# Kernel tuning notes

Measured on AMD Instinct MI355X. Metric: run time of the kernel, lower is better.

The kernel has to match this reference:

```python
import jax, jax.numpy as jnp
import numpy as np

D_MODEL = 768
D_FF = 2048
N_EXP = 8
TOP_K = 2


def setup_inputs() -> dict:
    key = jax.random.key(0)
    ks = jax.random.split(key, 8)
    s = 0.02
    inputs = jax.random.normal(ks[0], (4, 2048, D_MODEL), dtype=jnp.float32)
    gate_w = jax.random.normal(ks[1], (D_MODEL, N_EXP), dtype=jnp.float32) * s
    w1 = jax.random.normal(ks[2], (N_EXP, D_MODEL, D_FF), dtype=jnp.float32) * s
    w3 = jax.random.normal(ks[3], (N_EXP, D_MODEL, D_FF), dtype=jnp.float32) * s
    w2 = jax.random.normal(ks[4], (N_EXP, D_FF, D_MODEL), dtype=jnp.float32) * s
    sw1 = jax.random.normal(ks[5], (D_MODEL, D_FF), dtype=jnp.float32) * s
    sw3 = jax.random.normal(ks[6], (D_MODEL, D_FF), dtype=jnp.float32) * s
    sw2 = jax.random.normal(ks[7], (D_FF, D_MODEL), dtype=jnp.float32) * s
    return {"inputs": inputs, "gate_w": gate_w, "w1": w1, "w3": w3, "w2": w2,
            "sw1": sw1, "sw3": sw3, "sw2": sw2}


def _swiglu(x, wa, wb, wc):
    # silu(x @ wa) * (x @ wb) @ wc
    return (jax.nn.silu(x @ wa) * (x @ wb)) @ wc


def reference(inputs, gate_w, w1, w3, w2, sw1, sw3, sw2):
    B, T, D = inputs.shape
    x = inputs.reshape(-1, D)                      # [N, D], N = B*T
    logits = x @ gate_w                            # [N, E]
    topk_scores, topk_idx = jax.lax.top_k(logits, TOP_K)  # [N, K]
    probs = jax.nn.softmax(topk_scores.astype(jnp.float32), axis=-1).astype(inputs.dtype)
    # per-token per-expert combine weight: [N, E]
    one_hot = jax.nn.one_hot(topk_idx, N_EXP, dtype=probs.dtype)  # [N, K, E]
    comb = jnp.einsum('nk,nke->ne', probs, one_hot)               # [N, E]
    out = jnp.zeros_like(x)
    for e in range(N_EXP):  # fixed small expert loop
        out = out + comb[:, e:e + 1] * _swiglu(x, w1[e], w3[e], w2[e])
    out = out + _swiglu(x, sw1, sw3, sw2)
    return out.reshape(B, T, D)
```

## Files before the change

kernel.cpp:

```cpp
#include <hip/hip_runtime.h>
#include <hip/hip_bf16.h>

#define N_TOK 8192
#define DM 768
#define DFF 2048
#define NE 8
#define SHARED_BASE 17408
#define TOTAL_ROWS 25600

typedef __attribute__((ext_vector_type(8))) __bf16 bf16x8;
typedef __attribute__((ext_vector_type(4))) float f32x4;

__device__ __forceinline__ unsigned short f2bf(float f) {
  union { float f; unsigned u; } a; a.f = f;
  unsigned r = a.u + 0x7FFFu + ((a.u >> 16) & 1u);
  return (unsigned short)(r >> 16);
}

__device__ __forceinline__ void gload16(const void* g, void* l) {
  __builtin_amdgcn_global_load_lds((const __attribute__((address_space(1))) void*)g,
                                   (__attribute__((address_space(3))) void*)l, 16, 0, 0);
}


__global__ void cvt_x_kernel(const float4* __restrict__ src, ushort4* __restrict__ dst, int n4) {
  int stride = gridDim.x * blockDim.x;
  for (int i = blockIdx.x * blockDim.x + threadIdx.x; i < n4; i += stride) {
    float4 v = src[i];
    ushort4 o;
    o.x = f2bf(v.x); o.y = f2bf(v.y); o.z = f2bf(v.z); o.w = f2bf(v.w);
    dst[i] = o;
  }
}

__global__ void transpose_cvt_kernel(const float* __restrict__ src, unsigned short* __restrict__ dst,
                                     int R, int C) {
  __shared__ float tile[64][65];
  const float* s = src + (size_t)blockIdx.z * R * C;
  unsigned short* d = dst + (size_t)blockIdx.z * R * C;
  int c0 = blockIdx.x * 64, r0 = blockIdx.y * 64;
  int tx = threadIdx.x & 63, ty = threadIdx.x >> 6;
#pragma unroll
  for (int i = 0; i < 16; i++) {
    int row = i * 4 + ty;
    tile[row][tx] = s[(size_t)(r0 + row) * C + c0 + tx];
  }
  __syncthreads();
#pragma unroll
  for (int i = 0; i < 16; i++) {
    int row = i * 4 + ty;
    d[(size_t)(c0 + row) * R + r0 + tx] = f2bf(tile[tx][row]);
  }
}

__global__ __launch_bounds__(256) void gate_kernel(
    const float* __restrict__ x, const float* __restrict__ gw,
    float* __restrict__ probs, int* __restrict__ idxo) {
  __shared__ float gws[8][768];
  const int tid = threadIdx.x;
  for (int i = tid; i < DM * 2; i += 256) {
    float4 v = ((const float4*)gw)[i];
    int dd = i >> 1;
    int e0 = (i & 1) * 4;
    gws[e0 + 0][dd] = v.x; gws[e0 + 1][dd] = v.y;
    gws[e0 + 2][dd] = v.z; gws[e0 + 3][dd] = v.w;
  }
  __syncthreads();
  const int lane = tid & 63, wv = tid >> 6;
  const int tok0 = blockIdx.x * 16 + wv * 4;
  for (int i = 0; i < 4; i++) {
    const int n = tok0 + i;
    const float* xr = x + (size_t)n * DM;
    float xv[12];
#pragma unroll
    for (int it = 0; it < 12; it++) xv[it] = xr[it * 64 + lane];
    double acc[8];
#pragma unroll
    for (int e = 0; e < 8; e++) {
      double a = 0.0;
#pragma unroll
      for (int it = 0; it < 12; it++) a += (double)xv[it] * (double)gws[e][it * 64 + lane];
      acc[e] = a;
    }
#pragma unroll
    for (int off = 32; off > 0; off >>= 1)
#pragma unroll
      for (int e = 0; e < 8; e++) acc[e] += __shfl_xor(acc[e], off);
    if (lane == 0) {
      int e0 = 0; double v0 = acc[0];
#pragma unroll
      for (int e = 1; e < 8; e++) if (acc[e] > v0) { v0 = acc[e]; e0 = e; }
      int e1 = -1; double v1 = -1e300;
#pragma unroll
      for (int e = 0; e < 8; e++) if (e != e0 && acc[e] > v1) { v1 = acc[e]; e1 = e; }
      double p0 = 1.0 / (1.0 + exp(v1 - v0));
      probs[n * 2 + 0] = (float)p0;
      probs[n * 2 + 1] = (float)(1.0 - p0);
      idxo[n * 2 + 0] = e0;
      idxo[n * 2 + 1] = e1;
    }
  }
}

__global__ __launch_bounds__(256) void route_kernel(
    const int* __restrict__ idxo, const float* __restrict__ probs,
    int* __restrict__ cnt, int* __restrict__ offs,
    int* __restrict__ list, float* __restrict__ pslot) {
  __shared__ int lcnt[256][8];
  __shared__ int lstart[256][8];
  __shared__ int base[8];
  const int t = threadIdx.x;
#pragma unroll
  for (int e = 0; e < 8; e++) lcnt[t][e] = 0;
  __syncthreads();
  const int i0 = t * 64;
  for (int j = 0; j < 64; j++) {
    int e = idxo[i0 + j];
    lcnt[t][e]++;
  }
  __syncthreads();
  if (t < 8) {
    int run = 0;
    for (int tt = 0; tt < 256; tt++) { lstart[tt][t] = run; run += lcnt[tt][t]; }
    base[t] = run;
  }
  __syncthreads();
  if (t == 0) {
    int cum = 0;
    for (int e = 0; e < 8; e++) {
      int tot = base[e];
      cnt[e] = tot; offs[e] = cum;
      base[e] = cum;
      cum += (tot + 127) & ~127;
    }
    offs[8] = cum;
  }
  __syncthreads();
#pragma unroll
  for (int e = 0; e < 8; e++) lcnt[t][e] = base[e] + lstart[t][e];
  for (int j = 0; j < 64; j++) {
    int i = i0 + j;
    int e = idxo[i];
    int pos = lcnt[t][e]++;
    list[pos] = i >> 1;
    pslot[pos] = probs[i];
  }
}

__global__ __launch_bounds__(256, 2) void gemm1_kernel(
    const char* __restrict__ xb,
    const char* __restrict__ w1T,
    const char* __restrict__ w3T,
    const char* __restrict__ sw1T,
    const char* __restrict__ sw3T,
    const int* __restrict__ list, const int* __restrict__ cnt, const int* __restrict__ offs,
    unsigned short* __restrict__ Hb)
{
  __shared__ unsigned short Al[128 * 64];
  __shared__ unsigned short B1l[64 * 64];
  __shared__ unsigned short B3l[64 * 64];

  const int by = blockIdx.y;
  const int f0 = blockIdx.x * 64;
  const int tid = threadIdx.x;
  const int lane = tid & 63;
  const int wv = tid >> 6;
  const int wm = wv >> 1, wn = wv & 1;
  const int wflat = tid & ~63;

  const char *w1p, *w3p;
  int base_slot, tbase, cnt_e, offs_e = 0;
  const bool is_shared = (by >= 512);
  if (!is_shared) {
    int e = by >> 6, t = by & 63;
    cnt_e = cnt[e];
    if (t * 128 >= cnt_e) return;
    offs_e = offs[e];
    base_slot = offs_e + t * 128;
    tbase = t * 128;
    w1p = w1T + (size_t)e * DFF * DM * 2;
    w3p = w3T + (size_t)e * DFF * DM * 2;
  } else {
    int t = by - 512;
    base_slot = SHARED_BASE + t * 128;
    tbase = t * 128;
    cnt_e = 1 << 30;
    w1p = sw1T; w3p = sw3T;
  }

  const int brow = tid >> 3;
  const int bcol = tid & 7;

  size_t abase[4];
#pragma unroll
  for (int it = 0; it < 4; it++) {
    int row = it * 32 + brow;
    int tok;
    if (is_shared) tok = tbase + row;
    else {
      int ie = tbase + row;
      if (ie >= cnt_e) ie = cnt_e - 1;
      tok = list[offs_e + ie];
    }
    abase[it] = (size_t)tok * (DM * 2) + (size_t)((bcol ^ (row & 7)) << 4);
  }
  size_t bbase[2];
#pragma unroll
  for (int it = 0; it < 2; it++) {
    int row = it * 32 + brow;
    bbase[it] = (size_t)(f0 + row) * (DM * 2) + (size_t)((bcol ^ (row & 7)) << 4);
  }

  f32x4 acc1[4][2], acc3[4][2];
  const f32x4 z4 = {0.f, 0.f, 0.f, 0.f};
#pragma unroll
  for (int mi = 0; mi < 4; mi++)
#pragma unroll
    for (int ni = 0; ni < 2; ni++) { acc1[mi][ni] = z4; acc3[mi][ni] = z4; }

  const int ml = lane & 15, kg = lane >> 4;

  for (int ks = 0; ks < 12; ks++) {
#pragma unroll
    for (int it = 0; it < 4; it++)
      gload16(xb + abase[it] + ks * 128, (char*)Al + (size_t)((it * 256 + wflat) * 16));
#pragma unroll
    for (int it = 0; it < 2; it++) {
      gload16(w1p + bbase[it] + ks * 128, (char*)B1l + (size_t)((it * 256 + wflat) * 16));
      gload16(w3p + bbase[it] + ks * 128, (char*)B3l + (size_t)((it * 256 + wflat) * 16));
    }
    __syncthreads();
#pragma unroll
    for (int kk = 0; kk < 2; kk++) {
      const int kblk = kk * 4 + kg;
      bf16x8 af[4], b1f[2], b3f[2];
#pragma unroll
      for (int mi = 0; mi < 4; mi++) {
        int m = wm * 64 + mi * 16 + ml;
        af[mi] = *(const bf16x8*)((const char*)Al + m * 128 + ((kblk ^ (ml & 7)) << 4));
      }
#pragma unroll
      for (int ni = 0; ni < 2; ni++) {
        int nn = wn * 32 + ni * 16 + ml;
        int boff = nn * 128 + ((kblk ^ (ml & 7)) << 4);
        b1f[ni] = *(const bf16x8*)((const char*)B1l + boff);
        b3f[ni] = *(const bf16x8*)((const char*)B3l + boff);
      }
#pragma unroll
      for (int mi = 0; mi < 4; mi++)
#pragma unroll
        for (int ni = 0; ni < 2; ni++) {
          acc1[mi][ni] = __builtin_amdgcn_mfma_f32_16x16x32_bf16(af[mi], b1f[ni], acc1[mi][ni], 0, 0, 0);
          acc3[mi][ni] = __builtin_amdgcn_mfma_f32_16x16x32_bf16(af[mi], b3f[ni], acc3[mi][ni], 0, 0, 0);
        }
    }
    __syncthreads();
  }

#pragma unroll
  for (int mi = 0; mi < 4; mi++) {
#pragma unroll
    for (int ni = 0; ni < 2; ni++) {
#pragma unroll
      for (int r = 0; r < 4; r++) {
        int row = wm * 64 + mi * 16 + (lane >> 4) * 4 + r;
        int col = f0 + wn * 32 + ni * 16 + ml;
        float h1 = acc1[mi][ni][r], h3 = acc3[mi][ni][r];
        float s = h1 / (1.0f + expf(-h1));
        Hb[(size_t)(base_slot + row) * DFF + col] = f2bf(s * h3);
      }
    }
  }
}

__global__ __launch_bounds__(256, 2) void gemm2_kernel(
    const char* __restrict__ Hb,
    const char* __restrict__ w2T,
    const char* __restrict__ sw2T,
    const int* __restrict__ list, const int* __restrict__ cnt, const int* __restrict__ offs,
    const float* __restrict__ pslot,
    float* __restrict__ out, int shared_pass)
{
  __shared__ unsigned short Al[128 * 64];
  __shared__ unsigned short Bl[128 * 64];

  const int by = blockIdx.y;
  const int d0 = blockIdx.x * 128;
  const int tid = threadIdx.x;
  const int lane = tid & 63;
  const int wv = tid >> 6;
  const int wm = wv >> 1, wn = wv & 1;
  const int wflat = tid & ~63;

  const char* w2p;
  int base_slot, offs_e = 0, tbase, cnt_e;
  if (!shared_pass) {
    int e = by >> 6, t = by & 63;
    cnt_e = cnt[e];
    if (t * 128 >= cnt_e) return;
    offs_e = offs[e];
    base_slot = offs_e + t * 128;
    tbase = t * 128;
    w2p = w2T + (size_t)e * DM * DFF * 2;
  } else {
    int t = by;
    base_slot = SHARED_BASE + t * 128;
    tbase = t * 128;
    cnt_e = 1 << 30;
    w2p = sw2T;
  }

  const int brow = tid >> 3, bcol = tid & 7;
  size_t abase[4], bbase[4];
#pragma unroll
  for (int it = 0; it < 4; it++) {
    int row = it * 32 + brow;
    abase[it] = (size_t)(base_slot + row) * (DFF * 2) + (size_t)((bcol ^ (row & 7)) << 4);
    bbase[it] = (size_t)(d0 + row) * (DFF * 2) + (size_t)((bcol ^ (row & 7)) << 4);
  }

  f32x4 acc[4][4];
  const f32x4 z4 = {0.f, 0.f, 0.f, 0.f};
#pragma unroll
  for (int mi = 0; mi < 4; mi++)
#pragma unroll
    for (int ni = 0; ni < 4; ni++) acc[mi][ni] = z4;

  const int ml = lane & 15, kg = lane >> 4;

  for (int ks = 0; ks < 32; ks++) {
#pragma unroll
    for (int it = 0; it < 4; it++) {
      gload16(Hb + abase[it] + ks * 128, (char*)Al + (size_t)((it * 256 + wflat) * 16));
      gload16(w2p + bbase[it] + ks * 128, (char*)Bl + (size_t)((it * 256 + wflat) * 16));
    }
    __syncthreads();
#pragma unroll
    for (int kk = 0; kk < 2; kk++) {
      const int kblk = kk * 4 + kg;
      bf16x8 af[4], bf[4];
#pragma unroll
      for (int mi = 0; mi < 4; mi++) {
        int m = wm * 64 + mi * 16 + ml;
        af[mi] = *(const bf16x8*)((const char*)Al + m * 128 + ((kblk ^ (ml & 7)) << 4));
      }
#pragma unroll
      for (int ni = 0; ni < 4; ni++) {
        int nn = wn * 64 + ni * 16 + ml;
        bf[ni] = *(const bf16x8*)((const char*)Bl + nn * 128 + ((kblk ^ (ml & 7)) << 4));
      }
#pragma unroll
      for (int mi = 0; mi < 4; mi++)
#pragma unroll
        for (int ni = 0; ni < 4; ni++)
          acc[mi][ni] = __builtin_amdgcn_mfma_f32_16x16x32_bf16(af[mi], bf[ni], acc[mi][ni], 0, 0, 0);
    }
    __syncthreads();
  }

#pragma unroll
  for (int mi = 0; mi < 4; mi++) {
#pragma unroll
    for (int r = 0; r < 4; r++) {
      int row = wm * 64 + mi * 16 + (lane >> 4) * 4 + r;
      int ie = tbase + row;
      if (!shared_pass && ie >= cnt_e) continue;
      int tok; float p;
      if (shared_pass) { tok = tbase + row; p = 1.0f; }
      else { int slot = offs_e + ie; tok = list[slot]; p = pslot[slot]; }
      float* orow = out + (size_t)tok * DM + d0;
#pragma unroll
      for (int ni = 0; ni < 4; ni++) {
        int col = wn * 64 + ni * 16 + ml;
        float v = p * acc[mi][ni][r];
        if (shared_pass) orow[col] = v;
        else atomicAdd(&orow[col], v);
      }
    }
  }
}


extern "C" void kernel_launch(void* const* d_in, const int* in_sizes, int n_in,
                              void* d_out, int out_size, void* d_ws, size_t ws_size,
                              hipStream_t stream) {
  const float* x   = (const float*)d_in[0];
  const float* gw  = (const float*)d_in[1];
  const float* w1  = (const float*)d_in[2];
  const float* w3  = (const float*)d_in[3];
  const float* w2  = (const float*)d_in[4];
  const float* sw1 = (const float*)d_in[5];
  const float* sw3 = (const float*)d_in[6];
  const float* sw2 = (const float*)d_in[7];
  float* out = (float*)d_out;
  char* ws = (char*)d_ws;

  char* xb    = ws;
  char* w1T   = xb    + 12582912;
  char* w3T   = w1T   + 25165824;
  char* w2T   = w3T   + 25165824;
  char* sw1T  = w2T   + 25165824;
  char* sw3T  = sw1T  + 3145728;
  char* sw2T  = sw3T  + 3145728;
  char* Hb    = sw2T  + 3145728;
  char* probs = Hb    + 104857600;
  char* idxo  = probs + 65536;
  char* lst   = idxo  + 65536;
  char* psl   = lst   + 69632;
  char* cntb  = psl   + 69632;
  char* curb  = cntb  + 64;
  char* offb  = curb  + 64;

  cvt_x_kernel<<<2048, 256, 0, stream>>>((const float4*)x, (ushort4*)xb, N_TOK * DM / 4);
  transpose_cvt_kernel<<<dim3(32, 12, 8), 256, 0, stream>>>(w1, (unsigned short*)w1T, DM, DFF);
  transpose_cvt_kernel<<<dim3(32, 12, 8), 256, 0, stream>>>(w3, (unsigned short*)w3T, DM, DFF);
  transpose_cvt_kernel<<<dim3(12, 32, 8), 256, 0, stream>>>(w2, (unsigned short*)w2T, DFF, DM);
  transpose_cvt_kernel<<<dim3(32, 12, 1), 256, 0, stream>>>(sw1, (unsigned short*)sw1T, DM, DFF);
  transpose_cvt_kernel<<<dim3(32, 12, 1), 256, 0, stream>>>(sw3, (unsigned short*)sw3T, DM, DFF);
  transpose_cvt_kernel<<<dim3(12, 32, 1), 256, 0, stream>>>(sw2, (unsigned short*)sw2T, DFF, DM);

  gate_kernel<<<512, 256, 0, stream>>>(x, gw, (float*)probs, (int*)idxo);
  route_kernel<<<1, 256, 0, stream>>>((const int*)idxo, (const float*)probs,
                                      (int*)cntb, (int*)offb, (int*)lst, (float*)psl);

  gemm1_kernel<<<dim3(32, 576), 256, 0, stream>>>(xb, w1T, w3T, sw1T, sw3T,
      (const int*)lst, (const int*)cntb, (const int*)offb, (unsigned short*)Hb);

  gemm2_kernel<<<dim3(6, 64), 256, 0, stream>>>(Hb, w2T, sw2T, (const int*)lst, (const int*)cntb,
      (const int*)offb, (const float*)psl, out, 1);
  gemm2_kernel<<<dim3(6, 512), 256, 0, stream>>>(Hb, w2T, sw2T, (const int*)lst, (const int*)cntb,
      (const int*)offb, (const float*)psl, out, 0);
}
```

Measured before the change: 440.7 us.

## Enlarge GEMM tiles to 512 threads, double-buffer LDS, merge shared-expert pass

```diff
diff --git a/kernel.cpp b/kernel.cpp
--- a/kernel.cpp
+++ b/kernel.cpp
@@ -147,7 +147,7 @@
   }
 }
 
-__global__ __launch_bounds__(256, 2) void gemm1_kernel(
+__global__ __launch_bounds__(512, 2) void gemm1_kernel(
     const char* __restrict__ xb,
     const char* __restrict__ w1T,
     const char* __restrict__ w3T,
@@ -156,45 +156,44 @@
     const int* __restrict__ list, const int* __restrict__ cnt, const int* __restrict__ offs,
     unsigned short* __restrict__ Hb)
 {
-  __shared__ unsigned short Al[128 * 64];
-  __shared__ unsigned short B1l[64 * 64];
-  __shared__ unsigned short B3l[64 * 64];
+  __shared__ __attribute__((aligned(128))) unsigned char lds[131072];
 
   const int by = blockIdx.y;
-  const int f0 = blockIdx.x * 64;
+  const int f0 = blockIdx.x * 128;
   const int tid = threadIdx.x;
   const int lane = tid & 63;
   const int wv = tid >> 6;
-  const int wm = wv >> 1, wn = wv & 1;
-  const int wflat = tid & ~63;
+  const int wm = wv >> 1;
+  const int wn = wv & 1;
+  const int ml = lane & 15, kg = lane >> 4;
 
   const char *w1p, *w3p;
-  int base_slot, tbase, cnt_e, offs_e = 0;
-  const bool is_shared = (by >= 512);
+  int base_slot, tbase, cnt_e, cnt_pad = 1 << 30, offs_e = 0;
+  const bool is_shared = (by >= 256);
   if (!is_shared) {
-    int e = by >> 6, t = by & 63;
+    int e = by >> 5, t = by & 31;
     cnt_e = cnt[e];
-    if (t * 128 >= cnt_e) return;
+    if (t * 256 >= cnt_e) return;
+    cnt_pad = (cnt_e + 127) & ~127;
     offs_e = offs[e];
-    base_slot = offs_e + t * 128;
-    tbase = t * 128;
+    base_slot = offs_e + t * 256;
+    tbase = t * 256;
     w1p = w1T + (size_t)e * DFF * DM * 2;
     w3p = w3T + (size_t)e * DFF * DM * 2;
   } else {
-    int t = by - 512;
-    base_slot = SHARED_BASE + t * 128;
-    tbase = t * 128;
+    int t = by - 256;
+    base_slot = SHARED_BASE + t * 256;
+    tbase = t * 256;
     cnt_e = 1 << 30;
     w1p = sw1T; w3p = sw3T;
   }
 
-  const int brow = tid >> 3;
-  const int bcol = tid & 7;
-
+  const int srow = tid >> 3;
+  const int schk = tid & 7;
   size_t abase[4];
 #pragma unroll
   for (int it = 0; it < 4; it++) {
-    int row = it * 32 + brow;
+    int row = it * 64 + srow;
     int tok;
     if (is_shared) tok = tbase + row;
     else {
@@ -202,121 +201,130 @@
       if (ie >= cnt_e) ie = cnt_e - 1;
       tok = list[offs_e + ie];
     }
-    abase[it] = (size_t)tok * (DM * 2) + (size_t)((bcol ^ (row & 7)) << 4);
-  }
-  size_t bbase[2];
-#pragma unroll
-  for (int it = 0; it < 2; it++) {
-    int row = it * 32 + brow;
-    bbase[it] = (size_t)(f0 + row) * (DM * 2) + (size_t)((bcol ^ (row & 7)) << 4);
-  }
-
-  f32x4 acc1[4][2], acc3[4][2];
+    abase[it] = (size_t)tok * (DM * 2) + (size_t)((schk ^ (row & 7)) << 4);
+  }
+  const char* bptr[4];
+#pragma unroll
+  for (int it = 0; it < 4; it++) {
+    const char* wp = (it & 1) ? w3p : w1p;
+    int frow = f0 + ((it >> 1) << 6) + srow;
+    bptr[it] = wp + (size_t)frow * (DM * 2) + (size_t)((schk ^ (srow & 7)) << 4);
+  }
+
+  f32x4 acc[4][8];
   const f32x4 z4 = {0.f, 0.f, 0.f, 0.f};
 #pragma unroll
   for (int mi = 0; mi < 4; mi++)
 #pragma unroll
-    for (int ni = 0; ni < 2; ni++) { acc1[mi][ni] = z4; acc3[mi][ni] = z4; }
-
-  const int ml = lane & 15, kg = lane >> 4;
-
+    for (int nj = 0; nj < 8; nj++) acc[mi][nj] = z4;
+
+#define G1_STAGE(ks, b) {                                                        \
+    char* Ab_ = (char*)lds + (b) * 65536;                                        \
+    char* Bb_ = Ab_ + 32768;                                                     \
+    _Pragma("unroll")                                                            \
+    for (int it = 0; it < 4; it++)                                               \
+      gload16(xb + abase[it] + (ks) * 128, Ab_ + (it * 512 + tid) * 16);         \
+    _Pragma("unroll")                                                            \
+    for (int it = 0; it < 4; it++)                                               \
+      gload16(bptr[it] + (ks) * 128, Bb_ + (it * 512 + tid) * 16);               \
+  }
+
+  G1_STAGE(0, 0);
+  __syncthreads();
+  int cur = 0;
   for (int ks = 0; ks < 12; ks++) {
-#pragma unroll
-    for (int it = 0; it < 4; it++)
-      gload16(xb + abase[it] + ks * 128, (char*)Al + (size_t)((it * 256 + wflat) * 16));
-#pragma unroll
-    for (int it = 0; it < 2; it++) {
-      gload16(w1p + bbase[it] + ks * 128, (char*)B1l + (size_t)((it * 256 + wflat) * 16));
-      gload16(w3p + bbase[it] + ks * 128, (char*)B3l + (size_t)((it * 256 + wflat) * 16));
-    }
-    __syncthreads();
+    if (ks < 11) G1_STAGE(ks + 1, cur ^ 1);
+    const char* Ab = (const char*)lds + cur * 65536;
+    const char* Bb = Ab + 32768;
 #pragma unroll
     for (int kk = 0; kk < 2; kk++) {
       const int kblk = kk * 4 + kg;
-      bf16x8 af[4], b1f[2], b3f[2];
-#pragma unroll
-      for (int mi = 0; mi < 4; mi++) {
-        int m = wm * 64 + mi * 16 + ml;
-        af[mi] = *(const bf16x8*)((const char*)Al + m * 128 + ((kblk ^ (ml & 7)) << 4));
+      const int chk = (kblk ^ (ml & 7)) << 4;
+      bf16x8 af[4], bfr[8];
+#pragma unroll
+      for (int mi = 0; mi < 4; mi++)
+        af[mi] = *(const bf16x8*)(Ab + (wm * 64 + mi * 16 + ml) * 128 + chk);
+#pragma unroll
+      for (int nj = 0; nj < 8; nj++)
+        bfr[nj] = *(const bf16x8*)(Bb + (wn * 128 + nj * 16 + ml) * 128 + chk);
+#pragma unroll
+      for (int mi = 0; mi < 4; mi++)
+#pragma unroll
+        for (int nj = 0; nj < 8; nj++)
+          acc[mi][nj] = __builtin_amdgcn_mfma_f32_16x16x32_bf16(af[mi], bfr[nj], acc[mi][nj], 0, 0, 0);
+    }
+    __syncthreads();
+    cur ^= 1;
+  }
+
+#pragma unroll
+  for (int mi = 0; mi < 4; mi++) {
+#pragma unroll
+    for (int r = 0; r < 4; r++) {
+      int row = wm * 64 + mi * 16 + (lane >> 4) * 4 + r;
+      if (!is_shared && tbase + row >= cnt_pad) continue;
+      size_t hrow = (size_t)(base_slot + row) * DFF;
+#pragma unroll
+      for (int nj = 0; nj < 4; nj++) {
+        float h1 = acc[mi][nj][r], h3 = acc[mi][nj + 4][r];
+        float s = h1 / (1.0f + expf(-h1));
+        Hb[hrow + f0 + wn * 64 + nj * 16 + ml] = f2bf(s * h3);
       }
-#pragma unroll
-      for (int ni = 0; ni < 2; ni++) {
-        int nn = wn * 32 + ni * 16 + ml;
-        int boff = nn * 128 + ((kblk ^ (ml & 7)) << 4);
-        b1f[ni] = *(const bf16x8*)((const char*)B1l + boff);
-        b3f[ni] = *(const bf16x8*)((const char*)B3l + boff);
-      }
-#pragma unroll
-      for (int mi = 0; mi < 4; mi++)
-#pragma unroll
-        for (int ni = 0; ni < 2; ni++) {
-          acc1[mi][ni] = __builtin_amdgcn_mfma_f32_16x16x32_bf16(af[mi], b1f[ni], acc1[mi][ni], 0, 0, 0);
-          acc3[mi][ni] = __builtin_amdgcn_mfma_f32_16x16x32_bf16(af[mi], b3f[ni], acc3[mi][ni], 0, 0, 0);
-        }
-    }
-    __syncthreads();
-  }
-
-#pragma unroll
-  for (int mi = 0; mi < 4; mi++) {
-#pragma unroll
-    for (int ni = 0; ni < 2; ni++) {
-#pragma unroll
-      for (int r = 0; r < 4; r++) {
-        int row = wm * 64 + mi * 16 + (lane >> 4) * 4 + r;
-        int col = f0 + wn * 32 + ni * 16 + ml;
-        float h1 = acc1[mi][ni][r], h3 = acc3[mi][ni][r];
-        float s = h1 / (1.0f + expf(-h1));
-        Hb[(size_t)(base_slot + row) * DFF + col] = f2bf(s * h3);
-      }
-    }
-  }
-}
-
-__global__ __launch_bounds__(256, 2) void gemm2_kernel(
+    }
+  }
+#undef G1_STAGE
+}
+
+__global__ __launch_bounds__(512, 2) void gemm2_kernel(
     const char* __restrict__ Hb,
     const char* __restrict__ w2T,
     const char* __restrict__ sw2T,
     const int* __restrict__ list, const int* __restrict__ cnt, const int* __restrict__ offs,
     const float* __restrict__ pslot,
-    float* __restrict__ out, int shared_pass)
+    float* __restrict__ out)
 {
-  __shared__ unsigned short Al[128 * 64];
-  __shared__ unsigned short Bl[128 * 64];
+  __shared__ __attribute__((aligned(128))) unsigned char lds[98304];
 
   const int by = blockIdx.y;
   const int d0 = blockIdx.x * 128;
   const int tid = threadIdx.x;
   const int lane = tid & 63;
   const int wv = tid >> 6;
-  const int wm = wv >> 1, wn = wv & 1;
-  const int wflat = tid & ~63;
+  const int wm = wv >> 1;
+  const int wn = wv & 1;
+  const int ml = lane & 15, kg = lane >> 4;
 
   const char* w2p;
   int base_slot, offs_e = 0, tbase, cnt_e;
-  if (!shared_pass) {
-    int e = by >> 6, t = by & 63;
+  const bool is_shared = (by >= 256);
+  if (!is_shared) {
+    int e = by >> 5, t = by & 31;
     cnt_e = cnt[e];
-    if (t * 128 >= cnt_e) return;
+    if (t * 256 >= cnt_e) return;
     offs_e = offs[e];
-    base_slot = offs_e + t * 128;
-    tbase = t * 128;
+    base_slot = offs_e + t * 256;
+    tbase = t * 256;
     w2p = w2T + (size_t)e * DM * DFF * 2;
   } else {
-    int t = by;
-    base_slot = SHARED_BASE + t * 128;
-    tbase = t * 128;
+    int t = by - 256;
+    base_slot = SHARED_BASE + t * 256;
+    tbase = t * 256;
     cnt_e = 1 << 30;
     w2p = sw2T;
   }
 
-  const int brow = tid >> 3, bcol = tid & 7;
-  size_t abase[4], bbase[4];
+  const int srow = tid >> 3, schk = tid & 7;
+  size_t abase[4];
 #pragma unroll
   for (int it = 0; it < 4; it++) {
-    int row = it * 32 + brow;
-    abase[it] = (size_t)(base_slot + row) * (DFF * 2) + (size_t)((bcol ^ (row & 7)) << 4);
-    bbase[it] = (size_t)(d0 + row) * (DFF * 2) + (size_t)((bcol ^ (row & 7)) << 4);
+    int row = it * 64 + srow;
+    abase[it] = (size_t)(base_slot + row) * (DFF * 2) + (size_t)((schk ^ (row & 7)) << 4);
+  }
+  size_t bbase[2];
+#pragma unroll
+  for (int it = 0; it < 2; it++) {
+    int row = it * 64 + srow;
+    bbase[it] = (size_t)(d0 + row) * (DFF * 2) + (size_t)((schk ^ (row & 7)) << 4);
   }
 
   f32x4 acc[4][4];
@@ -324,38 +332,45 @@
 #pragma unroll
   for (int mi = 0; mi < 4; mi++)
 #pragma unroll
-    for (int ni = 0; ni < 4; ni++) acc[mi][ni] = z4;
-
-  const int ml = lane & 15, kg = lane >> 4;
-
+    for (int nj = 0; nj < 4; nj++) acc[mi][nj] = z4;
+
+#define G2_STAGE(ks, b) {                                                        \
+    char* Ab_ = (char*)lds + (b) * 49152;                                        \
+    char* Bb_ = Ab_ + 32768;                                                     \
+    _Pragma("unroll")                                                            \
+    for (int it = 0; it < 4; it++)                                               \
+      gload16(Hb + abase[it] + (ks) * 128, Ab_ + (it * 512 + tid) * 16);         \
+    _Pragma("unroll")                                                            \
+    for (int it = 0; it < 2; it++)                                               \
+      gload16(w2p + bbase[it] + (ks) * 128, Bb_ + (it * 512 + tid) * 16);        \
+  }
+
+  G2_STAGE(0, 0);
+  __syncthreads();
+  int cur = 0;
   for (int ks = 0; ks < 32; ks++) {
-#pragma unroll
-    for (int it = 0; it < 4; it++) {
-      gload16(Hb + abase[it] + ks * 128, (char*)Al + (size_t)((it * 256 + wflat) * 16));
-      gload16(w2p + bbase[it] + ks * 128, (char*)Bl + (size_t)((it * 256 + wflat) * 16));
-    }
-    __syncthreads();
+    if (ks < 31) G2_STAGE(ks + 1, cur ^ 1);
+    const char* Ab = (const char*)lds + cur * 49152;
+    const char* Bb = Ab + 32768;
 #pragma unroll
     for (int kk = 0; kk < 2; kk++) {
       const int kblk = kk * 4 + kg;
-      bf16x8 af[4], bf[4];
-#pragma unroll
-      for (int mi = 0; mi < 4; mi++) {
-        int m = wm * 64 + mi * 16 + ml;
-        af[mi] = *(const bf16x8*)((const char*)Al + m * 128 + ((kblk ^ (ml & 7)) << 4));
-      }
-#pragma unroll
-      for (int ni = 0; ni < 4; ni++) {
-        int nn = wn * 64 + ni * 16 + ml;
-        bf[ni] = *(const bf16x8*)((const char*)Bl + nn * 128 + ((kblk ^ (ml & 7)) << 4));
-      }
+      const int chk = (kblk ^ (ml & 7)) << 4;
+      bf16x8 af[4], bfr[4];
 #pragma unroll
       for (int mi = 0; mi < 4; mi++)
-#pragma unroll
-        for (int ni = 0; ni < 4; ni++)
-          acc[mi][ni] = __builtin_amdgcn_mfma_f32_16x16x32_bf16(af[mi], bf[ni], acc[mi][ni], 0, 0, 0);
+        af[mi] = *(const bf16x8*)(Ab + (wm * 64 + mi * 16 + ml) * 128 + chk);
+#pragma unroll
+      for (int nj = 0; nj < 4; nj++)
+        bfr[nj] = *(const bf16x8*)(Bb + (wn * 64 + nj * 16 + ml) * 128 + chk);
+#pragma unroll
+      for (int mi = 0; mi < 4; mi++)
+#pragma unroll
+        for (int nj = 0; nj < 4; nj++)
+          acc[mi][nj] = __builtin_amdgcn_mfma_f32_16x16x32_bf16(af[mi], bfr[nj], acc[mi][nj], 0, 0, 0);
     }
     __syncthreads();
+    cur ^= 1;
   }
 
 #pragma unroll
@@ -364,20 +379,17 @@
     for (int r = 0; r < 4; r++) {
       int row = wm * 64 + mi * 16 + (lane >> 4) * 4 + r;
       int ie = tbase + row;
-      if (!shared_pass && ie >= cnt_e) continue;
+      if (!is_shared && ie >= cnt_e) continue;
       int tok; float p;
-      if (shared_pass) { tok = tbase + row; p = 1.0f; }
+      if (is_shared) { tok = tbase + row; p = 1.0f; }
       else { int slot = offs_e + ie; tok = list[slot]; p = pslot[slot]; }
       float* orow = out + (size_t)tok * DM + d0;
 #pragma unroll
-      for (int ni = 0; ni < 4; ni++) {
-        int col = wn * 64 + ni * 16 + ml;
-        float v = p * acc[mi][ni][r];
-        if (shared_pass) orow[col] = v;
-        else atomicAdd(&orow[col], v);
-      }
-    }
-  }
+      for (int nj = 0; nj < 4; nj++)
+        atomicAdd(&orow[wn * 64 + nj * 16 + ml], p * acc[mi][nj][r]);
+    }
+  }
+#undef G2_STAGE
 }
 
 
@@ -408,8 +420,9 @@
   char* lst   = idxo  + 65536;
   char* psl   = lst   + 69632;
   char* cntb  = psl   + 69632;
-  char* curb  = cntb  + 64;
-  char* offb  = curb  + 64;
+  char* offb  = cntb  + 64;
+
+  (void)hipMemsetAsync(out, 0, (size_t)out_size * 4, stream);
 
   cvt_x_kernel<<<2048, 256, 0, stream>>>((const float4*)x, (ushort4*)xb, N_TOK * DM / 4);
   transpose_cvt_kernel<<<dim3(32, 12, 8), 256, 0, stream>>>(w1, (unsigned short*)w1T, DM, DFF);
@@ -423,11 +436,9 @@
   route_kernel<<<1, 256, 0, stream>>>((const int*)idxo, (const float*)probs,
                                       (int*)cntb, (int*)offb, (int*)lst, (float*)psl);
 
-  gemm1_kernel<<<dim3(32, 576), 256, 0, stream>>>(xb, w1T, w3T, sw1T, sw3T,
+  gemm1_kernel<<<dim3(16, 288), 512, 0, stream>>>(xb, w1T, w3T, sw1T, sw3T,
       (const int*)lst, (const int*)cntb, (const int*)offb, (unsigned short*)Hb);
 
-  gemm2_kernel<<<dim3(6, 64), 256, 0, stream>>>(Hb, w2T, sw2T, (const int*)lst, (const int*)cntb,
-      (const int*)offb, (const float*)psl, out, 1);
-  gemm2_kernel<<<dim3(6, 512), 256, 0, stream>>>(Hb, w2T, sw2T, (const int*)lst, (const int*)cntb,
-      (const int*)offb, (const float*)psl, out, 0);
-}
+  gemm2_kernel<<<dim3(6, 288), 512, 0, stream>>>(Hb, w2T, sw2T, (const int*)lst, (const int*)cntb,
+      (const int*)offb, (const float*)psl, out);
+}
```

Result: slower. 458.4 us (+4.0%).

## Replace atomic scatter in expert down-projection with slot buffer plus combine kernel

Applied to the files above, without the earlier changes.

```diff
diff --git a/kernel.cpp b/kernel.cpp
--- a/kernel.cpp
+++ b/kernel.cpp
@@ -103,9 +103,9 @@
 }
 
 __global__ __launch_bounds__(256) void route_kernel(
-    const int* __restrict__ idxo, const float* __restrict__ probs,
+    const int* __restrict__ idxo,
     int* __restrict__ cnt, int* __restrict__ offs,
-    int* __restrict__ list, float* __restrict__ pslot) {
+    int* __restrict__ list, int* __restrict__ slt) {
   __shared__ int lcnt[256][8];
   __shared__ int lstart[256][8];
   __shared__ int base[8];
@@ -143,7 +143,7 @@
     int e = idxo[i];
     int pos = lcnt[t][e]++;
     list[pos] = i >> 1;
-    pslot[pos] = probs[i];
+    slt[i] = pos;
   }
 }
 
@@ -277,9 +277,9 @@
     const char* __restrict__ Hb,
     const char* __restrict__ w2T,
     const char* __restrict__ sw2T,
-    const int* __restrict__ list, const int* __restrict__ cnt, const int* __restrict__ offs,
-    const float* __restrict__ pslot,
-    float* __restrict__ out, int shared_pass)
+    const int* __restrict__ cnt, const int* __restrict__ offs,
+    float* __restrict__ Ob,
+    float* __restrict__ out)
 {
   __shared__ unsigned short Al[128 * 64];
   __shared__ unsigned short Bl[128 * 64];
@@ -293,17 +293,17 @@
   const int wflat = tid & ~63;
 
   const char* w2p;
-  int base_slot, offs_e = 0, tbase, cnt_e;
-  if (!shared_pass) {
+  int base_slot, tbase, cnt_e;
+  const bool is_shared = (by >= 512);
+  if (!is_shared) {
     int e = by >> 6, t = by & 63;
     cnt_e = cnt[e];
     if (t * 128 >= cnt_e) return;
-    offs_e = offs[e];
-    base_slot = offs_e + t * 128;
+    base_slot = offs[e] + t * 128;
     tbase = t * 128;
     w2p = w2T + (size_t)e * DM * DFF * 2;
   } else {
-    int t = by;
+    int t = by - 512;
     base_slot = SHARED_BASE + t * 128;
     tbase = t * 128;
     cnt_e = 1 << 30;
@@ -338,7 +338,7 @@
 #pragma unroll
     for (int kk = 0; kk < 2; kk++) {
       const int kblk = kk * 4 + kg;
-      bf16x8 af[4], bf[4];
+      bf16x8 af[4], bfr[4];
 #pragma unroll
       for (int mi = 0; mi < 4; mi++) {
         int m = wm * 64 + mi * 16 + ml;
@@ -347,13 +347,13 @@
 #pragma unroll
       for (int ni = 0; ni < 4; ni++) {
         int nn = wn * 64 + ni * 16 + ml;
-        bf[ni] = *(const bf16x8*)((const char*)Bl + nn * 128 + ((kblk ^ (ml & 7)) << 4));
+        bfr[ni] = *(const bf16x8*)((const char*)Bl + nn * 128 + ((kblk ^ (ml & 7)) << 4));
       }
 #pragma unroll
       for (int mi = 0; mi < 4; mi++)
 #pragma unroll
         for (int ni = 0; ni < 4; ni++)
-          acc[mi][ni] = __builtin_amdgcn_mfma_f32_16x16x32_bf16(af[mi], bf[ni], acc[mi][ni], 0, 0, 0);
+          acc[mi][ni] = __builtin_amdgcn_mfma_f32_16x16x32_bf16(af[mi], bfr[ni], acc[mi][ni], 0, 0, 0);
     }
     __syncthreads();
   }
@@ -363,21 +363,30 @@
 #pragma unroll
     for (int r = 0; r < 4; r++) {
       int row = wm * 64 + mi * 16 + (lane >> 4) * 4 + r;
-      int ie = tbase + row;
-      if (!shared_pass && ie >= cnt_e) continue;
-      int tok; float p;
-      if (shared_pass) { tok = tbase + row; p = 1.0f; }
-      else { int slot = offs_e + ie; tok = list[slot]; p = pslot[slot]; }
-      float* orow = out + (size_t)tok * DM + d0;
-#pragma unroll
-      for (int ni = 0; ni < 4; ni++) {
-        int col = wn * 64 + ni * 16 + ml;
-        float v = p * acc[mi][ni][r];
-        if (shared_pass) orow[col] = v;
-        else atomicAdd(&orow[col], v);
-      }
-    }
-  }
+      float* orow = is_shared ? (out + (size_t)(tbase + row) * DM + d0)
+                              : (Ob + (size_t)(base_slot + row) * DM + d0);
+#pragma unroll
+      for (int ni = 0; ni < 4; ni++)
+        orow[wn * 64 + ni * 16 + ml] = acc[mi][ni][r];
+    }
+  }
+}
+
+__global__ __launch_bounds__(192) void combine_kernel(
+    const float4* __restrict__ Ob4, const int* __restrict__ slt,
+    const float* __restrict__ probs, float4* __restrict__ out4) {
+  const int n = blockIdx.x;
+  const int t = threadIdx.x;
+  const int s0 = slt[2 * n], s1 = slt[2 * n + 1];
+  const float p0 = probs[2 * n], p1 = probs[2 * n + 1];
+  float4 a = out4[(size_t)n * 192 + t];
+  float4 b = Ob4[(size_t)s0 * 192 + t];
+  float4 c = Ob4[(size_t)s1 * 192 + t];
+  a.x += p0 * b.x + p1 * c.x;
+  a.y += p0 * b.y + p1 * c.y;
+  a.z += p0 * b.z + p1 * c.z;
+  a.w += p0 * b.w + p1 * c.w;
+  out4[(size_t)n * 192 + t] = a;
 }
 
 
@@ -395,21 +404,22 @@
   float* out = (float*)d_out;
   char* ws = (char*)d_ws;
 
-  char* xb    = ws;
-  char* w1T   = xb    + 12582912;
-  char* w3T   = w1T   + 25165824;
-  char* w2T   = w3T   + 25165824;
-  char* sw1T  = w2T   + 25165824;
-  char* sw3T  = sw1T  + 3145728;
-  char* sw2T  = sw3T  + 3145728;
-  char* Hb    = sw2T  + 3145728;
-  char* probs = Hb    + 104857600;
-  char* idxo  = probs + 65536;
-  char* lst   = idxo  + 65536;
-  char* psl   = lst   + 69632;
-  char* cntb  = psl   + 69632;
-  char* curb  = cntb  + 64;
-  char* offb  = curb  + 64;
+  char* xb   = ws;
+  char* w2T  = xb + 12582912;
+  char* sw2T = w2T + 25165824;
+  char* U    = sw2T + 3145728;
+  char* w1T  = U;
+  char* w3T  = w1T + 25165824;
+  char* sw1T = w3T + 25165824;
+  char* sw3T = sw1T + 3145728;
+  char* Ob   = U;
+  char* Hb   = U + 56623104;
+  char* probs= Hb + 104857600;
+  char* idxo = probs + 65536;
+  char* lst  = idxo + 65536;
+  char* slt  = lst + 69632;
+  char* cntb = slt + 69632;
+  char* offb = cntb + 64;
 
   cvt_x_kernel<<<2048, 256, 0, stream>>>((const float4*)x, (ushort4*)xb, N_TOK * DM / 4);
   transpose_cvt_kernel<<<dim3(32, 12, 8), 256, 0, stream>>>(w1, (unsigned short*)w1T, DM, DFF);
@@ -420,14 +430,15 @@
   transpose_cvt_kernel<<<dim3(12, 32, 1), 256, 0, stream>>>(sw2, (unsigned short*)sw2T, DFF, DM);
 
   gate_kernel<<<512, 256, 0, stream>>>(x, gw, (float*)probs, (int*)idxo);
-  route_kernel<<<1, 256, 0, stream>>>((const int*)idxo, (const float*)probs,
-                                      (int*)cntb, (int*)offb, (int*)lst, (float*)psl);
+  route_kernel<<<1, 256, 0, stream>>>((const int*)idxo,
+                                      (int*)cntb, (int*)offb, (int*)lst, (int*)slt);
 
   gemm1_kernel<<<dim3(32, 576), 256, 0, stream>>>(xb, w1T, w3T, sw1T, sw3T,
       (const int*)lst, (const int*)cntb, (const int*)offb, (unsigned short*)Hb);
 
-  gemm2_kernel<<<dim3(6, 64), 256, 0, stream>>>(Hb, w2T, sw2T, (const int*)lst, (const int*)cntb,
-      (const int*)offb, (const float*)psl, out, 1);
-  gemm2_kernel<<<dim3(6, 512), 256, 0, stream>>>(Hb, w2T, sw2T, (const int*)lst, (const int*)cntb,
-      (const int*)offb, (const float*)psl, out, 0);
-}
+  gemm2_kernel<<<dim3(6, 576), 256, 0, stream>>>(Hb, w2T, sw2T,
+      (const int*)cntb, (const int*)offb, (float*)Ob, out);
+
+  combine_kernel<<<N_TOK, 192, 0, stream>>>((const float4*)Ob, (const int*)slt,
+                                            (const float*)probs, (float4*)out);
+}
```

Result: no change. 433.6 us (-1.6%).
